# Performance work log

Measured on AMD Instinct MI355X. Metric: run time of the kernel, lower is better.

Reference implementation:

```python
import jax, jax.numpy as jnp
import numpy as np
from jax import lax

DIM = 256
POS = 32
RATIO = 4
LN_EPS = 1e-5


def _layernorm(x, g, b):
    m = x.mean(-1, keepdims=True)
    v = ((x - m) ** 2).mean(-1, keepdims=True)
    return (x - m) * lax.rsqrt(v + LN_EPS) * g + b


def _pos_embed(pos, h, w):
    # pos: [1, C, POS, POS] -> bilinear (align_corners=False / half-pixel) -> [1, h*w, C]
    p = jax.image.resize(pos, (1, pos.shape[1], h, w), method='bilinear')
    return p.transpose(0, 2, 3, 1).reshape(1, h * w, pos.shape[1])


def _scan_branch(u, ln_g, ln_b, Wf, bf, Ww, bw, Wo, bo):
    # u: [B, N, C]. Pooled LN context -> concat gates -> gated linear recurrence.
    c = _layernorm(u.mean(1), ln_g, ln_b)                       # [B, C]
    z = jnp.concatenate([u, jnp.broadcast_to(c[:, None, :], u.shape)], -1)
    d = jax.nn.softplus(z @ Wf + bf)
    g = jax.nn.sigmoid(z @ Ww + bw)
    o = jax.nn.sigmoid(z @ Wo + bo)
    a = jnp.exp(-d)
    b = (1.0 - a) * (g * u)

    def step(s, t):
        a_t, b_t, o_t, u_t = t
        s = a_t * s + b_t
        return s, o_t * s + (1.0 - o_t) * u_t

    xs = tuple(jnp.swapaxes(v, 0, 1) for v in (a, b, o, u))     # [N, B, C]
    s0 = jnp.zeros((u.shape[0], u.shape[2]), u.dtype)
    _, y = lax.scan(step, s0, xs)
    return jnp.swapaxes(y, 0, 1)                                # [B, N, C]


def setup_inputs() -> dict:
    key = jax.random.key(0)
    ks = jax.random.split(key, 32)
    d = DIM

    def W(k, i, o, s=0.02):
        return (jax.random.normal(k, (i, o), jnp.float32) * s)

    inp = {
        'x': jax.random.normal(ks[0], (8, d, 64, 64), jnp.float32),
        'Wt': W(ks[1], d, d), 'bt': jnp.zeros((d,), jnp.float32),
        'pos_fine': jax.random.normal(ks[2], (1, d, POS, POS), jnp.float32) * 0.02,
        'pos_glob': jax.random.normal(ks[3], (1, d, POS, POS), jnp.float32) * 0.02,
        'ln_g': jnp.ones((d,), jnp.float32), 'ln_b': jnp.zeros((d,), jnp.float32),
        'Wf': W(ks[4], 2 * d, d), 'bf': jnp.zeros((d,), jnp.float32),
        'Ww': W(ks[5], 2 * d, d), 'bw': jnp.zeros((d,), jnp.float32),
        'Wo': W(ks[6], 2 * d, d), 'bo': jnp.zeros((d,), jnp.float32),
        'Wr': W(ks[7], 3 * d, d), 'br': jnp.zeros((d,), jnp.float32),
        'Wgi': W(ks[8], 3 * d, d), 'bgi': jnp.zeros((d,), jnp.float32),
        'dw_w': jax.random.normal(ks[9], (d, 1, 3, 3), jnp.float32) * 0.1,
        'dw_b': jnp.zeros((d,), jnp.float32),
        'Wl': W(ks[10], d, d), 'bl': jnp.zeros((d,), jnp.float32),
        'Wlf': W(ks[11], 2 * d, d), 'blf': jnp.zeros((d,), jnp.float32),
        'Wout': W(ks[12], d, d), 'bout': jnp.zeros((d,), jnp.float32),
    }
    return inp


def reference(x, Wt, bt, pos_fine, pos_glob, ln_g, ln_b, Wf, bf, Ww, bw, Wo, bo,
              Wr, br, Wgi, bgi, dw_w, dw_b, Wl, bl, Wlf, blf, Wout, bout):
    bsz, c, h, w = x.shape
    gate_params = (ln_g, ln_b, Wf, bf, Ww, bw, Wo, bo)

    # fine sequence: token proj + interpolated learnable pos
    seq = x.transpose(0, 2, 3, 1).reshape(bsz, h * w, c)
    u = seq @ Wt + bt + _pos_embed(pos_fine, h, w)

    # bidirectional gated scan
    y_f = _scan_branch(u, *gate_params)
    y_b = jnp.flip(_scan_branch(jnp.flip(u, 1), *gate_params), 1)
    rho = jax.nn.sigmoid(jnp.concatenate([u, y_f, y_b], -1) @ Wr + br)
    y = rho * y_f + (1.0 - rho) * y_b

    # global branch: exact avg pool (H,W divisible by RATIO) -> scan -> upsample
    gh, gw = h // RATIO, w // RATIO
    x_g = x.reshape(bsz, c, gh, RATIO, gw, RATIO).mean((3, 5))
    seq_g = x_g.transpose(0, 2, 3, 1).reshape(bsz, gh * gw, c)
    u_g = seq_g @ Wt + bt + _pos_embed(pos_glob, gh, gw)
    y_g = _scan_branch(u_g, *gate_params)
    y_g_map = y_g.reshape(bsz, gh, gw, c).transpose(0, 3, 1, 2)
    y_g_up = jax.image.resize(y_g_map, (bsz, c, h, w), method='bilinear')
    y_g_seq = y_g_up.transpose(0, 2, 3, 1).reshape(bsz, h * w, c)

    lam = jax.nn.sigmoid(jnp.concatenate([y, y_g_seq, u], -1) @ Wgi + bgi)
    z = y + lam * y_g_seq

    # local depthwise conv branch
    v_map = lax.conv_general_dilated(x, dw_w, (1, 1), 'SAME',
                                     feature_group_count=c) + dw_b[None, :, None, None]
    v = v_map.transpose(0, 2, 3, 1).reshape(bsz, h * w, c) @ Wl + bl
    eta = jax.nn.sigmoid(jnp.concatenate([v, z], -1) @ Wlf + blf)
    u_out = eta * v + (1.0 - eta) * z

    # 1x1 conv output proj + residual
    out_map = (u_out @ Wout + bout).reshape(bsz, h, w, c).transpose(0, 3, 1, 2)
    return x + out_map
```

## Files before the change

### kernel.cpp

```cpp
#include <hip/hip_runtime.h>
#include <cstddef>

#define B_  8
#define C_  256
#define H_  64
#define W_  64
#define HW_ 4096
#define NG_ 256

typedef unsigned short u16;
typedef __attribute__((ext_vector_type(8))) short short8;
typedef __attribute__((ext_vector_type(4))) float f32x4;

__device__ __forceinline__ float sigm(float v) { return 1.f / (1.f + expf(-v)); }

__device__ __forceinline__ u16 f2bf(float f) {
    union { float f; unsigned u; } x; x.f = f;
    unsigned r = x.u + 0x7fff + ((x.u >> 16) & 1);
    return (u16)(r >> 16);
}
__device__ __forceinline__ float bf2f(u16 h) {
    union { unsigned u; float f; } x; x.u = ((unsigned)h) << 16;
    return x.f;
}

__global__ __launch_bounds__(256) void prepw_k(
    const float* __restrict__ Wt, const float* __restrict__ Wf, const float* __restrict__ Ww,
    const float* __restrict__ Wo, const float* __restrict__ Wr, const float* __restrict__ Wgi,
    const float* __restrict__ Wl, const float* __restrict__ Wlf, const float* __restrict__ Wout,
    u16* __restrict__ Wpre)
{
    int s = blockIdx.z;
    const float* Wsrc; int rowoff = 0;
    switch (s) {
        case 0: Wsrc = Wt; break;
        case 1: Wsrc = Wf; break;
        case 2: Wsrc = Ww; break;
        case 3: Wsrc = Wo; break;
        case 4: case 5: case 6: Wsrc = Wr;  rowoff = (s - 4) * 256; break;
        case 7: case 8: case 9: Wsrc = Wgi; rowoff = (s - 7) * 256; break;
        case 10: Wsrc = Wl; break;
        case 11: case 12: Wsrc = Wlf; rowoff = (s - 11) * 256; break;
        default: Wsrc = Wout; break;
    }
    __shared__ float t[32][33];
    int k0 = blockIdx.y * 32, n0 = blockIdx.x * 32;
    int tx = threadIdx.x, ty = threadIdx.y;
#pragma unroll
    for (int i = 0; i < 32; i += 8)
        t[ty + i][tx] = Wsrc[(size_t)(rowoff + k0 + ty + i) * 256 + n0 + tx];
    __syncthreads();
    u16* op = Wpre + (size_t)s * 65536;
#pragma unroll
    for (int i = 0; i < 32; i += 8)
        op[(size_t)(n0 + ty + i) * 256 + k0 + tx] = f2bf(t[tx][ty + i]);
}

#define LDK 72
__global__ __launch_bounds__(256, 4) void gemm_bf16(
    const u16* __restrict__ A0, const u16* __restrict__ A1, const u16* __restrict__ A2,
    int nseg, const u16* __restrict__ Wpre, const float* __restrict__ bias,
    const float* __restrict__ pos, const float* __restrict__ aux0,
    const u16* __restrict__ auxb0, const u16* __restrict__ auxb1,
    float* __restrict__ out, u16* __restrict__ out2, int NTOK, int mode)
{
    __shared__ u16 Asm[64 * LDK];
    __shared__ u16 Bsm[128 * LDK];
    const int tid = threadIdx.x;
    const int lane = tid & 63, wave = tid >> 6;
    const int wm = wave & 1, wn = wave >> 1;
    const int m0 = blockIdx.x * 64, n0 = blockIdx.y * 128;
    const int l15 = lane & 15, lq = lane >> 4;

    f32x4 acc[2][4] = {};

    const int rowA = tid >> 2, kA = (tid & 3) * 16;
    const int rowB = tid >> 1, kB = (tid & 1) * 32;

    for (int seg = 0; seg < nseg; ++seg) {
        const u16* __restrict__ A = (seg == 0) ? A0 : ((seg == 1) ? A1 : A2);
        const u16* arow = A + (size_t)(m0 + rowA) * 256 + kA;
        const u16* wrow = Wpre + (size_t)seg * 65536 + (size_t)(n0 + rowB) * 256 + kB;

        for (int k0 = 0; k0 < 256; k0 += 64) {
            *(short8*)(&Asm[rowA * LDK + kA])     = *(const short8*)(arow + k0);
            *(short8*)(&Asm[rowA * LDK + kA + 8]) = *(const short8*)(arow + k0 + 8);
#pragma unroll
            for (int c = 0; c < 4; ++c)
                *(short8*)(&Bsm[rowB * LDK + kB + c * 8]) =
                    *(const short8*)(wrow + k0 + c * 8);
            __syncthreads();

#pragma unroll
            for (int ks = 0; ks < 2; ++ks) {
                short8 af[2], bfr[4];
#pragma unroll
                for (int i = 0; i < 2; ++i)
                    af[i] = *(const short8*)(&Asm[(wm * 32 + i * 16 + l15) * LDK + ks * 32 + lq * 8]);
#pragma unroll
                for (int j = 0; j < 4; ++j)
                    bfr[j] = *(const short8*)(&Bsm[(wn * 64 + j * 16 + l15) * LDK + ks * 32 + lq * 8]);
#pragma unroll
                for (int i = 0; i < 2; ++i)
#pragma unroll
                    for (int j = 0; j < 4; ++j)
                        acc[i][j] = __builtin_amdgcn_mfma_f32_16x16x32_bf16(
                            af[i], bfr[j], acc[i][j], 0, 0, 0);
            }
            __syncthreads();
        }
    }

#pragma unroll
    for (int i = 0; i < 2; ++i) {
        int mbase = m0 + wm * 32 + i * 16 + lq * 4;
#pragma unroll
        for (int j = 0; j < 4; ++j) {
            int n = n0 + wn * 64 + j * 16 + l15;
            if (mode == 9) {
                int b9 = mbase >> 12, hw = mbase & 4095;
                size_t oi = ((size_t)b9 * 256 + n) * 4096 + hw;
                float bn = bias[n];
                float4 xr = *(const float4*)(aux0 + oi);
                float4 res;
                res.x = xr.x + acc[i][j][0] + bn;
                res.y = xr.y + acc[i][j][1] + bn;
                res.z = xr.z + acc[i][j][2] + bn;
                res.w = xr.w + acc[i][j][3] + bn;
                *(float4*)(out + oi) = res;
                continue;
            }
            float bn = bias[n];
#pragma unroll
            for (int r = 0; r < 4; ++r) {
                int m = mbase + r;
                size_t idx = (size_t)m * 256 + n;
                float D = acc[i][j][r] + bn;
                if (mode == 1) {
                    float v = D + pos[(size_t)(m % NTOK) * 256 + n];
                    out[idx] = v; out2[idx] = f2bf(v);
                } else if (mode == 10) {
                    float v = D + pos[(size_t)(m % NTOK) * 256 + n];
                    out2[idx] = f2bf(v);
                } else if (mode == 11) {
                    float r_ = sigm(D);
                    out2[idx] = f2bf(r_ * bf2f(auxb0[idx]) + (1.f - r_) * bf2f(auxb1[idx]));
                } else if (mode == 6) {
                    float l = sigm(D);
                    out2[idx] = f2bf(bf2f(auxb1[idx]) + l * bf2f(auxb0[idx]));
                } else if (mode == 7) {
                    out2[idx] = f2bf(D);
                } else {
                    float e = sigm(D);
                    out2[idx] = f2bf(e * bf2f(auxb0[idx]) + (1.f - e) * bf2f(auxb1[idx]));
                }
            }
        }
    }
}

__global__ __launch_bounds__(256, 4) void gemm_gates3(
    const u16* __restrict__ A0, const u16* __restrict__ Wg, const float* __restrict__ cf,
    const u16* __restrict__ ubf, float* __restrict__ aF, float* __restrict__ bbF,
    u16* __restrict__ obf, int NTOK)
{
    __shared__ u16 Asm[64 * LDK];
    __shared__ u16 Bsm[3][64 * LDK];
    const int tid = threadIdx.x;
    const int lane = tid & 63, wave = tid >> 6;
    const int wm = wave & 1, wn = wave >> 1;
    const int m0 = blockIdx.x * 64, n0 = blockIdx.y * 64;
    const int l15 = lane & 15, lq = lane >> 4;

    f32x4 acc[3][2][2] = {};

    const int rowA = tid >> 2, kA = (tid & 3) * 16;
    const u16* arow = A0 + (size_t)(m0 + rowA) * 256 + kA;
    const u16* wrow = Wg + (size_t)(n0 + rowA) * 256 + kA;

    for (int k0 = 0; k0 < 256; k0 += 64) {
        *(short8*)(&Asm[rowA * LDK + kA])     = *(const short8*)(arow + k0);
        *(short8*)(&Asm[rowA * LDK + kA + 8]) = *(const short8*)(arow + k0 + 8);
#pragma unroll
        for (int ws = 0; ws < 3; ++ws) {
            const u16* wr = wrow + (size_t)ws * 65536 + k0;
            *(short8*)(&Bsm[ws][rowA * LDK + kA])     = *(const short8*)(wr);
            *(short8*)(&Bsm[ws][rowA * LDK + kA + 8]) = *(const short8*)(wr + 8);
        }
        __syncthreads();
#pragma unroll
        for (int ks = 0; ks < 2; ++ks) {
            short8 af[2];
#pragma unroll
            for (int i = 0; i < 2; ++i)
                af[i] = *(const short8*)(&Asm[(wm * 32 + i * 16 + l15) * LDK + ks * 32 + lq * 8]);
#pragma unroll
            for (int ws = 0; ws < 3; ++ws) {
                short8 bfr[2];
#pragma unroll
                for (int j = 0; j < 2; ++j)
                    bfr[j] = *(const short8*)(&Bsm[ws][(wn * 32 + j * 16 + l15) * LDK + ks * 32 + lq * 8]);
#pragma unroll
                for (int i = 0; i < 2; ++i)
#pragma unroll
                    for (int j = 0; j < 2; ++j)
                        acc[ws][i][j] = __builtin_amdgcn_mfma_f32_16x16x32_bf16(
                            af[i], bfr[j], acc[ws][i][j], 0, 0, 0);
            }
        }
        __syncthreads();
    }

#pragma unroll
    for (int i = 0; i < 2; ++i) {
        int mbase = m0 + wm * 32 + i * 16 + lq * 4;
        int bt_ = mbase / NTOK;
#pragma unroll
        for (int j = 0; j < 2; ++j) {
            int n = n0 + wn * 32 + j * 16 + l15;
            float cD = cf[((size_t)0 * B_ + bt_) * C_ + n];
            float cW = cf[((size_t)1 * B_ + bt_) * C_ + n];
            float cO = cf[((size_t)2 * B_ + bt_) * C_ + n];
#pragma unroll
            for (int r = 0; r < 4; ++r) {
                size_t idx = (size_t)(mbase + r) * 256 + n;
                float a_ = sigm(-(acc[0][i][j][r] + cD));
                float g_ = sigm(acc[1][i][j][r] + cW);
                float o_ = sigm(acc[2][i][j][r] + cO);
                float u_ = bf2f(ubf[idx]);
                aF[idx]  = a_;
                bbF[idx] = (1.f - a_) * g_ * u_;
                obf[idx] = f2bf(o_);
            }
        }
    }
}

__global__ __launch_bounds__(256) void transpose_bf_k(const float* __restrict__ in,
                                                      u16* __restrict__ outb)
{
    __shared__ float t[32][33];
    int b = blockIdx.z;
    int r0 = blockIdx.y * 32, c0 = blockIdx.x * 32;
    int tx = threadIdx.x, ty = threadIdx.y;
    const float* ip = in + (size_t)b * HW_ * C_;
    u16* op = outb + (size_t)b * HW_ * C_;
#pragma unroll
    for (int k = 0; k < 32; k += 8)
        t[ty + k][tx] = ip[(size_t)(r0 + ty + k) * HW_ + c0 + tx];
    __syncthreads();
#pragma unroll
    for (int k = 0; k < 32; k += 8)
        op[(size_t)(c0 + ty + k) * C_ + r0 + tx] = f2bf(t[tx][ty + k]);
}

__global__ __launch_bounds__(256) void dwconvt3_k(const float* __restrict__ x,
                                                  const float* __restrict__ dww,
                                                  const float* __restrict__ dwb,
                                                  u16* __restrict__ vseq)
{
    __shared__ float sx[32 * 384];
    __shared__ float sw[32 * 9];
    __shared__ float sb[32];
    const int t = threadIdx.x;
    const int l   = (blockIdx.x & 7) * 128 + (blockIdx.x >> 3);
    const int hch = l & 15;
    const int chb = (l >> 4) & 7;
    const int b   = l >> 7;
    const int r0 = chb * 32, h0 = hch * 4;

    for (int p = t; p < 288; p += 256) sw[p] = dww[(size_t)(r0 + p / 9) * 9 + p % 9];
    if (t < 32) sb[t] = dwb[r0 + t];

    const float* xb = x + (size_t)(b * 256 + r0) * 4096;
#pragma unroll
    for (int j = 0; j < 12; ++j) {
        int seg = j * 256 + t;
        int ch  = seg / 96;
        int r4  = seg - ch * 96;
        int rr  = r4 >> 4;
        int w4  = (r4 & 15) * 4;
        int hh  = h0 - 1 + rr;
        float4 v = make_float4(0.f, 0.f, 0.f, 0.f);
        if (hh >= 0 && hh <= 63)
            v = *(const float4*)(xb + (size_t)ch * 4096 + hh * 64 + w4);
        *(float4*)(&sx[seg * 4]) = v;
    }
    __syncthreads();

    const int w = t & 63, chq = t >> 6;
    float res[4][8];
#pragma unroll
    for (int i = 0; i < 8; ++i) {
        const int ch = chq * 8 + i;
        const float* cw = &sw[ch * 9];
        const float* bp = &sx[ch * 384 + w];
        float aa[4];
        aa[0] = aa[1] = aa[2] = aa[3] = sb[ch];
#pragma unroll
        for (int rr = 0; rr < 6; ++rr) {
            const float* rp = bp + rr * 64;
            float cc = rp[0];
            float lf = (w > 0)  ? rp[-1] : 0.f;
            float rt = (w < 63) ? rp[1]  : 0.f;
            if (rr < 4)            aa[rr]     += lf * cw[0] + cc * cw[1] + rt * cw[2];
            if (rr >= 1 && rr < 5) aa[rr - 1] += lf * cw[3] + cc * cw[4] + rt * cw[5];
            if (rr >= 2)           aa[rr - 2] += lf * cw[6] + cc * cw[7] + rt * cw[8];
        }
#pragma unroll
        for (int r = 0; r < 4; ++r) res[r][i] = aa[r];
    }

    size_t obase = ((size_t)b * HW_ + (size_t)(h0 * 64 + w)) * 256 + r0 + chq * 8;
#pragma unroll
    for (int r = 0; r < 4; ++r) {
        short8 v;
#pragma unroll
        for (int i = 0; i < 8; ++i) v[i] = (short)f2bf(res[r][i]);
        *(short8*)(vseq + obase + (size_t)r * 64 * 256) = v;
    }
}

__global__ __launch_bounds__(256) void pool_k(const float* __restrict__ x, u16* __restrict__ seqg)
{
    int b = blockIdx.x, c = blockIdx.y, ghw = threadIdx.x;
    int gh = ghw >> 4, gw = ghw & 15;
    const float* xp = x + ((size_t)b * C_ + c) * HW_;
    float s = 0.f;
#pragma unroll
    for (int dy = 0; dy < 4; ++dy)
#pragma unroll
        for (int dx = 0; dx < 4; ++dx)
            s += xp[(gh * 4 + dy) * W_ + gw * 4 + dx];
    seqg[((size_t)b * NG_ + ghw) * C_ + c] = f2bf(s * (1.f / 16.f));
}

__global__ __launch_bounds__(256) void posfine_k(const float* __restrict__ pf, float* __restrict__ posF)
{
    int hw = blockIdx.x, c = threadIdx.x;
    int h = hw >> 6, w = hw & 63;
    float fy = h * 0.5f - 0.25f, fx = w * 0.5f - 0.25f;
    int y0 = (int)floorf(fy); float wy = fy - (float)y0;
    int x0 = (int)floorf(fx); float wx = fx - (float)x0;
    int y0c = min(max(y0, 0), 31), y1c = min(max(y0 + 1, 0), 31);
    int x0c = min(max(x0, 0), 31), x1c = min(max(x0 + 1, 0), 31);
    const float* p = pf + (size_t)c * 1024;
    float v = (1.f - wy) * ((1.f - wx) * p[y0c * 32 + x0c] + wx * p[y0c * 32 + x1c])
            +        wy  * ((1.f - wx) * p[y1c * 32 + x0c] + wx * p[y1c * 32 + x1c]);
    posF[(size_t)hw * C_ + c] = v;
}

__global__ __launch_bounds__(256) void posglob_k(const float* __restrict__ pg, float* __restrict__ posG)
{
    int ghw = blockIdx.x, c = threadIdx.x;
    int gh = ghw >> 4, gw = ghw & 15;
    const float wt[4] = {0.125f, 0.375f, 0.375f, 0.125f};
    float wy[4], wx[4]; int jy[4], jx[4];
    float sy = 0.f, sx = 0.f;
#pragma unroll
    for (int k = 0; k < 4; ++k) {
        jy[k] = 2 * gh - 1 + k; jx[k] = 2 * gw - 1 + k;
        wy[k] = (jy[k] >= 0 && jy[k] < 32) ? wt[k] : 0.f; sy += wy[k];
        wx[k] = (jx[k] >= 0 && jx[k] < 32) ? wt[k] : 0.f; sx += wx[k];
    }
    const float* p = pg + (size_t)c * 1024;
    float acc = 0.f;
#pragma unroll
    for (int ky = 0; ky < 4; ++ky) {
        if (wy[ky] == 0.f) continue;
        float row = 0.f;
#pragma unroll
        for (int kx = 0; kx < 4; ++kx)
            if (wx[kx] != 0.f) row += wx[kx] * p[jy[ky] * 32 + jx[kx]];
        acc += wy[ky] * row;
    }
    posG[(size_t)ghw * C_ + c] = acc / (sy * sx);
}

__global__ __launch_bounds__(256) void upsample_k(const float* __restrict__ yg, u16* __restrict__ ygs)
{
    int b = blockIdx.x >> 12, hw = blockIdx.x & 4095, c = threadIdx.x;
    int h = hw >> 6, w = hw & 63;
    float fy = h * 0.25f - 0.375f, fx = w * 0.25f - 0.375f;
    int y0 = (int)floorf(fy); float wy = fy - (float)y0;
    int x0 = (int)floorf(fx); float wx = fx - (float)x0;
    int y0c = min(max(y0, 0), 15), y1c = min(max(y0 + 1, 0), 15);
    int x0c = min(max(x0, 0), 15), x1c = min(max(x0 + 1, 0), 15);
    const float* p = yg + (size_t)b * NG_ * C_ + c;
    float v = (1.f - wy) * ((1.f - wx) * p[(y0c * 16 + x0c) * C_] + wx * p[(y0c * 16 + x1c) * C_])
            +        wy  * ((1.f - wx) * p[(y1c * 16 + x0c) * C_] + wx * p[(y1c * 16 + x1c) * C_]);
    ygs[((size_t)b * HW_ + hw) * C_ + c] = f2bf(v);
}

__global__ __launch_bounds__(256) void meanpart_k(const float* __restrict__ u, float* __restrict__ part,
                                                  int Ntok, int chunkLen)
{
    int b = blockIdx.x, s = blockIdx.y, c = threadIdx.x;
    float acc = 0.f;
    for (int i = 0; i < chunkLen; ++i) {
        int t = s * chunkLen + i;
        acc += u[((size_t)b * Ntok + t) * C_ + c];
    }
    part[((size_t)b * gridDim.y + s) * C_ + c] = acc;
}

__global__ __launch_bounds__(256) void meanpart_bf_k(const u16* __restrict__ u, float* __restrict__ part,
                                                     int Ntok, int chunkLen)
{
    int b = blockIdx.x, s = blockIdx.y, c = threadIdx.x;
    float acc = 0.f;
    for (int i = 0; i < chunkLen; ++i) {
        int t = s * chunkLen + i;
        acc += bf2f(u[((size_t)b * Ntok + t) * C_ + c]);
    }
    part[((size_t)b * gridDim.y + s) * C_ + c] = acc;
}

__global__ __launch_bounds__(256) void ln_k(const float* __restrict__ part, int S, float invN,
                                            const float* __restrict__ g, const float* __restrict__ bta,
                                            float* __restrict__ cout)
{
    __shared__ float red[256];
    int c = threadIdx.x, b = blockIdx.x;
    float v = 0.f;
    for (int s = 0; s < S; ++s) v += part[((size_t)b * S + s) * C_ + c];
    v *= invN;
    red[c] = v; __syncthreads();
    for (int st = 128; st > 0; st >>= 1) { if (c < st) red[c] += red[c + st]; __syncthreads(); }
    float m = red[0] * (1.f / 256.f);
    __syncthreads();
    float d = v - m;
    red[c] = d * d; __syncthreads();
    for (int st = 128; st > 0; st >>= 1) { if (c < st) red[c] += red[c + st]; __syncthreads(); }
    float var = red[0] * (1.f / 256.f);
    cout[(size_t)b * C_ + c] = d * rsqrtf(var + 1e-5f) * g[c] + bta[c];
}

__global__ __launch_bounds__(256) void gatebias_k(const float* __restrict__ cvec,
    const float* __restrict__ Wf, const float* __restrict__ bf,
    const float* __restrict__ Ww, const float* __restrict__ bw,
    const float* __restrict__ Wo, const float* __restrict__ bo,
    float* __restrict__ outb)
{
    int n = threadIdx.x, b = blockIdx.x, gate = blockIdx.y;
    const float* Wm = (gate == 0) ? Wf : ((gate == 1) ? Ww : Wo);
    const float* bi = (gate == 0) ? bf : ((gate == 1) ? bw : bo);
    __shared__ float cs[256];
    cs[n] = cvec[(size_t)b * C_ + n];
    __syncthreads();
    float acc = bi[n];
    for (int k = 0; k < 256; ++k)
        acc += cs[k] * Wm[(size_t)(256 + k) * C_ + n];
    outb[((size_t)gate * B_ + b) * C_ + n] = acc;
}

__global__ __launch_bounds__(256) void scan_p1b(
    const float* __restrict__ a, const float* __restrict__ bb,
    float* __restrict__ AbF, float* __restrict__ BbF,
    float* __restrict__ AbB, float* __restrict__ BbB,
    int Ntok, int nchunk, int both)
{
    int c = threadIdx.x;
    int ch = blockIdx.x % nchunk;
    int b = blockIdx.x / nchunk;
    int CL = Ntok / nchunk;
    size_t base = ((size_t)b * Ntok + (size_t)ch * CL) * C_ + c;
    float sA = 1.f, sB = 0.f;
    for (int i = 0; i < CL; ++i) {
        float av = a[base + (size_t)i * C_];
        sB = av * sB + bb[base + (size_t)i * C_];
        sA *= av;
    }
    size_t o = ((size_t)b * nchunk + ch) * C_ + c;
    AbF[o] = sA; BbF[o] = sB;
    if (both) {
        sA = 1.f; sB = 0.f;
        for (int i = CL - 1; i >= 0; --i) {
            float av = a[base + (size_t)i * C_];
            sB = av * sB + bb[base + (size_t)i * C_];
            sA *= av;
        }
        size_t ob = ((size_t)b * nchunk + (nchunk - 1 - ch)) * C_ + c;
        AbB[ob] = sA; BbB[ob] = sB;
    }
}

__global__ __launch_bounds__(256) void scan_p2b(
    const float* __restrict__ AbF, const float* __restrict__ BbF, float* __restrict__ SbF,
    const float* __restrict__ AbB, const float* __restrict__ BbB, float* __restrict__ SbB,
    int nchunk, int both)
{
    int c = threadIdx.x, b = blockIdx.x;
    float s = 0.f;
    for (int ch = 0; ch < nchunk; ++ch) {
        size_t o = ((size_t)b * nchunk + ch) * C_ + c;
        SbF[o] = s;
        s = AbF[o] * s + BbF[o];
    }
    if (both) {
        s = 0.f;
        for (int ch = 0; ch < nchunk; ++ch) {
            size_t o = ((size_t)b * nchunk + ch) * C_ + c;
            SbB[o] = s;
            s = AbB[o] * s + BbB[o];
        }
    }
}

__global__ __launch_bounds__(256) void scan_p3b(
    const float* __restrict__ a, const float* __restrict__ bb,
    const u16* __restrict__ obf, const u16* __restrict__ ubf,
    const float* __restrict__ SbF, const float* __restrict__ SbB,
    float* __restrict__ yout, u16* __restrict__ ybfF, u16* __restrict__ ybfB,
    int Ntok, int nchunk, int both)
{
    int c = threadIdx.x;
    int ch = blockIdx.x % nchunk;
    int b = blockIdx.x / nchunk;
    int CL = Ntok / nchunk;
    size_t base = ((size_t)b * Ntok + (size_t)ch * CL) * C_ + c;
    float s = SbF[((size_t)b * nchunk + ch) * C_ + c];
    for (int i = 0; i < CL; ++i) {
        size_t idx = base + (size_t)i * C_;
        float av = a[idx];
        s = av * s + bb[idx];
        float ov = bf2f(obf[idx]);
        float y = ov * s + (1.f - ov) * bf2f(ubf[idx]);
        if (yout) yout[idx] = y;
        if (ybfF) ybfF[idx] = f2bf(y);
    }
    if (both) {
        float sb = SbB[((size_t)b * nchunk + (nchunk - 1 - ch)) * C_ + c];
        for (int i = CL - 1; i >= 0; --i) {
            size_t idx = base + (size_t)i * C_;
            float av = a[idx];
            sb = av * sb + bb[idx];
            float ov = bf2f(obf[idx]);
            ybfB[idx] = f2bf(ov * sb + (1.f - ov) * bf2f(ubf[idx]));
        }
    }
}

extern "C" void kernel_launch(void* const* d_in, const int* in_sizes, int n_in,
                              void* d_out, int out_size, void* d_ws, size_t ws_size,
                              hipStream_t stream)
{
    const float* x        = (const float*)d_in[0];
    const float* Wt       = (const float*)d_in[1];
    const float* bt       = (const float*)d_in[2];
    const float* pos_fine = (const float*)d_in[3];
    const float* pos_glob = (const float*)d_in[4];
    const float* ln_g     = (const float*)d_in[5];
    const float* ln_b     = (const float*)d_in[6];
    const float* Wf       = (const float*)d_in[7];
    const float* bf       = (const float*)d_in[8];
    const float* Ww       = (const float*)d_in[9];
    const float* bw       = (const float*)d_in[10];
    const float* Wo       = (const float*)d_in[11];
    const float* bo       = (const float*)d_in[12];
    const float* Wr       = (const float*)d_in[13];
    const float* br       = (const float*)d_in[14];
    const float* Wgi      = (const float*)d_in[15];
    const float* bgi      = (const float*)d_in[16];
    const float* dww      = (const float*)d_in[17];
    const float* dwb      = (const float*)d_in[18];
    const float* Wl       = (const float*)d_in[19];
    const float* bl       = (const float*)d_in[20];
    const float* Wlf      = (const float*)d_in[21];
    const float* blf      = (const float*)d_in[22];
    const float* Wout     = (const float*)d_in[23];
    const float* bout     = (const float*)d_in[24];
    float* out = (float*)d_out;

    float* w = (float*)d_ws;
    const size_t BNC = (size_t)B_ * HW_ * C_;
    float* bu  = w + 0 * BNC;
    float* ba  = w + 1 * BNC;
    float* bbb = w + 2 * BNC;
    float* bo_ = w + 3 * BNC;
    u16* bf1 = (u16*)(w + 4 * BNC);
    u16* bf2 = bf1 + BNC;
    u16* bf3 = bf2 + BNC;
    u16* bf4 = bf3 + BNC;
    u16* bf5 = bf4 + BNC;
    float* ext = w + 4 * BNC + 5 * (BNC / 2);
    float* posF = ext;  ext += (size_t)HW_ * C_;
    float* posG = ext;  ext += (size_t)NG_ * C_;
    float* part = ext;  ext += (size_t)B_ * 32 * C_;
    float* cln  = ext;  ext += (size_t)B_ * C_;
    float* cf   = ext;  ext += (size_t)3 * B_ * C_;
    float* ug   = ext;  ext += (size_t)B_ * NG_ * C_;
    float* ag   = ext;  ext += (size_t)B_ * NG_ * C_;
    float* bbg  = ext;  ext += (size_t)B_ * NG_ * C_;
    float* ygt  = ext;  ext += (size_t)B_ * NG_ * C_;
    float* chAF = ext;  ext += (size_t)B_ * 64 * C_;
    float* chBF = ext;  ext += (size_t)B_ * 64 * C_;
    float* chSF = ext;  ext += (size_t)B_ * 64 * C_;
    u16* seqg_bf = (u16*)ext;  ext += (size_t)B_ * NG_ * C_ / 2;
    u16* ug_bf   = (u16*)ext;  ext += (size_t)B_ * NG_ * C_ / 2;
    u16* og_bf   = (u16*)ext;  ext += (size_t)B_ * NG_ * C_ / 2;
    u16* Wpre    = (u16*)ext;
    float* chAB = bu;
    float* chBB = bu + (size_t)B_ * 64 * C_;
    float* chSB = bu + (size_t)2 * B_ * 64 * C_;
    u16* obf    = (u16*)bo_;

    const dim3 blk256(256);
    const dim3 blkT(32, 8);
    const dim3 gBig(B_ * HW_ / 64, 2);
    const dim3 gSml(B_ * NG_ / 64, 2);
    const dim3 gGateF(B_ * HW_ / 64, 4);
    const dim3 gGateG(B_ * NG_ / 64, 4);
    const size_t WS = 65536;
    const float *F0 = nullptr; const u16 *U0 = nullptr;
    float *FW = nullptr; u16 *UW = nullptr;

    prepw_k<<<dim3(8, 8, 14), blkT, 0, stream>>>(Wt, Wf, Ww, Wo, Wr, Wgi, Wl, Wlf, Wout, Wpre);

    transpose_bf_k<<<dim3(HW_ / 32, C_ / 32, B_), blkT, 0, stream>>>(x, bf1);
    posfine_k<<<HW_, blk256, 0, stream>>>(pos_fine, posF);
    gemm_bf16<<<gBig, blk256, 0, stream>>>(bf1, U0, U0, 1, Wpre + 0 * WS, bt,
        posF, F0, U0, U0, FW, bf2, HW_, 10);

    pool_k<<<dim3(B_, C_), blk256, 0, stream>>>(x, seqg_bf);
    posglob_k<<<NG_, blk256, 0, stream>>>(pos_glob, posG);
    gemm_bf16<<<gSml, blk256, 0, stream>>>(seqg_bf, U0, U0, 1, Wpre + 0 * WS, bt,
        posG, F0, U0, U0, ug, ug_bf, NG_, 1);
    meanpart_k<<<dim3(B_, 8), blk256, 0, stream>>>(ug, part, NG_, 32);
    ln_k<<<B_, blk256, 0, stream>>>(part, 8, 1.f / NG_, ln_g, ln_b, cln);
    gatebias_k<<<dim3(B_, 3), blk256, 0, stream>>>(cln, Wf, bf, Ww, bw, Wo, bo, cf);
    gemm_gates3<<<gGateG, blk256, 0, stream>>>(ug_bf, Wpre + 1 * WS, cf, ug_bf,
        ag, bbg, og_bf, NG_);
    scan_p1b<<<B_ * 16, blk256, 0, stream>>>(ag, bbg, chAF, chBF, FW, FW, NG_, 16, 0);
    scan_p2b<<<B_, blk256, 0, stream>>>(chAF, chBF, chSF, F0, F0, FW, 16, 0);
    scan_p3b<<<B_ * 16, blk256, 0, stream>>>(ag, bbg, og_bf, ug_bf, chSF, F0,
        ygt, UW, UW, NG_, 16, 0);
    upsample_k<<<B_ * HW_, blk256, 0, stream>>>(ygt, bf5);

    meanpart_bf_k<<<dim3(B_, 32), blk256, 0, stream>>>(bf2, part, HW_, 128);
    ln_k<<<B_, blk256, 0, stream>>>(part, 32, 1.f / HW_, ln_g, ln_b, cln);
    gatebias_k<<<dim3(B_, 3), blk256, 0, stream>>>(cln, Wf, bf, Ww, bw, Wo, bo, cf);
    gemm_gates3<<<gGateF, blk256, 0, stream>>>(bf2, Wpre + 1 * WS, cf, bf2,
        ba, bbb, obf, HW_);
    scan_p1b<<<B_ * 64, blk256, 0, stream>>>(ba, bbb, chAF, chBF, chAB, chBB, HW_, 64, 1);
    scan_p2b<<<B_, blk256, 0, stream>>>(chAF, chBF, chSF, chAB, chBB, chSB, 64, 1);
    scan_p3b<<<B_ * 64, blk256, 0, stream>>>(ba, bbb, obf, bf2, chSF, chSB,
        FW, bf1, bf3, HW_, 64, 1);

    gemm_bf16<<<gBig, blk256, 0, stream>>>(bf2, bf1, bf3, 3, Wpre + 4 * WS, br,
        F0, F0, bf1, bf3, FW, bf4, HW_, 11);

    gemm_bf16<<<gBig, blk256, 0, stream>>>(bf4, bf5, bf2, 3, Wpre + 7 * WS, bgi,
        F0, F0, bf5, bf4, FW, bf1, HW_, 6);

    dwconvt3_k<<<dim3(1024), blk256, 0, stream>>>(x, dww, dwb, bf3);
    gemm_bf16<<<gBig, blk256, 0, stream>>>(bf3, U0, U0, 1, Wpre + 10 * WS, bl,
        F0, F0, U0, U0, FW, bf2, HW_, 7);
    gemm_bf16<<<gBig, blk256, 0, stream>>>(bf2, bf1, U0, 2, Wpre + 11 * WS, blf,
        F0, F0, bf2, bf1, FW, bf3, HW_, 8);

    gemm_bf16<<<gBig, blk256, 0, stream>>>(bf3, U0, U0, 1, Wpre + 13 * WS, bout,
        F0, x, U0, U0, out, UW, HW_, 9);
}
```

Measured before the change: 641.8 us.

## Raise scan chunk count and parallelize forward/backward carry pass with prefetch

The fine-scale scan now uses 256 chunks instead of 64, so phases 1 and 3 launch four times as many blocks with shorter serial chains. The carry-propagation kernel runs the forward and backward directions in two halves of a 512-thread block and software-prefetches chunk summaries in groups of 8. The chunk buffers are moved into a larger scratch region. In exchange, the serial phase-2 chain becomes longer, and the new kernel assumes nchunk is a multiple of 8.

```diff
diff --git a/kernel.cpp b/kernel.cpp
--- a/kernel.cpp
+++ b/kernel.cpp
@@ -485,25 +485,42 @@
     }
 }
 
-__global__ __launch_bounds__(256) void scan_p2b(
+__global__ __launch_bounds__(512) void scan_p2c(
     const float* __restrict__ AbF, const float* __restrict__ BbF, float* __restrict__ SbF,
     const float* __restrict__ AbB, const float* __restrict__ BbB, float* __restrict__ SbB,
     int nchunk, int both)
 {
-    int c = threadIdx.x, b = blockIdx.x;
+    const int c = threadIdx.x & 255, half = threadIdx.x >> 8, b = blockIdx.x;
+    if (half && !both) return;
+    const float* __restrict__ Ap = half ? AbB : AbF;
+    const float* __restrict__ Bp = half ? BbB : BbF;
+    float* __restrict__       Sp = half ? SbB : SbF;
+    const size_t base = (size_t)b * nchunk * C_ + c;
+    float a0[8], b0[8], a1[8], b1[8];
+#pragma unroll
+    for (int j = 0; j < 8; ++j) {
+        a0[j] = Ap[base + (size_t)j * C_];
+        b0[j] = Bp[base + (size_t)j * C_];
+    }
     float s = 0.f;
-    for (int ch = 0; ch < nchunk; ++ch) {
-        size_t o = ((size_t)b * nchunk + ch) * C_ + c;
-        SbF[o] = s;
-        s = AbF[o] * s + BbF[o];
-    }
-    if (both) {
-        s = 0.f;
-        for (int ch = 0; ch < nchunk; ++ch) {
-            size_t o = ((size_t)b * nchunk + ch) * C_ + c;
-            SbB[o] = s;
-            s = AbB[o] * s + BbB[o];
-        }
+    const int nb = nchunk >> 3;
+    for (int t = 0; t < nb; ++t) {
+        const size_t nbase = base + (size_t)(t + 1) * 8 * C_;
+        if (t + 1 < nb) {
+#pragma unroll
+            for (int j = 0; j < 8; ++j) {
+                a1[j] = Ap[nbase + (size_t)j * C_];
+                b1[j] = Bp[nbase + (size_t)j * C_];
+            }
+        }
+        const size_t cbase = base + (size_t)t * 8 * C_;
+#pragma unroll
+        for (int j = 0; j < 8; ++j) {
+            Sp[cbase + (size_t)j * C_] = s;
+            s = a0[j] * s + b0[j];
+        }
+#pragma unroll
+        for (int j = 0; j < 8; ++j) { a0[j] = a1[j]; b0[j] = b1[j]; }
     }
 }
 
@@ -593,16 +610,17 @@
     float* ag   = ext;  ext += (size_t)B_ * NG_ * C_;
     float* bbg  = ext;  ext += (size_t)B_ * NG_ * C_;
     float* ygt  = ext;  ext += (size_t)B_ * NG_ * C_;
-    float* chAF = ext;  ext += (size_t)B_ * 64 * C_;
-    float* chBF = ext;  ext += (size_t)B_ * 64 * C_;
-    float* chSF = ext;  ext += (size_t)B_ * 64 * C_;
     u16* seqg_bf = (u16*)ext;  ext += (size_t)B_ * NG_ * C_ / 2;
     u16* ug_bf   = (u16*)ext;  ext += (size_t)B_ * NG_ * C_ / 2;
     u16* og_bf   = (u16*)ext;  ext += (size_t)B_ * NG_ * C_ / 2;
     u16* Wpre    = (u16*)ext;
-    float* chAB = bu;
-    float* chBB = bu + (size_t)B_ * 64 * C_;
-    float* chSB = bu + (size_t)2 * B_ * 64 * C_;
+    const size_t CHS = (size_t)B_ * 256 * C_;
+    float* chAF = bu + 0 * CHS;
+    float* chBF = bu + 1 * CHS;
+    float* chSF = bu + 2 * CHS;
+    float* chAB = bu + 3 * CHS;
+    float* chBB = bu + 4 * CHS;
+    float* chSB = bu + 5 * CHS;
     u16* obf    = (u16*)bo_;
 
     const dim3 blk256(256);
@@ -612,6 +630,8 @@
     const dim3 gGateF(B_ * HW_ / 64, 4);
     const dim3 gGateG(B_ * NG_ / 64, 4);
     const size_t WS = 65536;
+    const int NCH_F = 256;
+    const int NCH_G = 16;
     const float *F0 = nullptr; const u16 *U0 = nullptr;
     float *FW = nullptr; u16 *UW = nullptr;
 
@@ -631,10 +651,10 @@
     gatebias_k<<<dim3(B_, 3), blk256, 0, stream>>>(cln, Wf, bf, Ww, bw, Wo, bo, cf);
     gemm_gates3<<<gGateG, blk256, 0, stream>>>(ug_bf, Wpre + 1 * WS, cf, ug_bf,
         ag, bbg, og_bf, NG_);
-    scan_p1b<<<B_ * 16, blk256, 0, stream>>>(ag, bbg, chAF, chBF, FW, FW, NG_, 16, 0);
-    scan_p2b<<<B_, blk256, 0, stream>>>(chAF, chBF, chSF, F0, F0, FW, 16, 0);
-    scan_p3b<<<B_ * 16, blk256, 0, stream>>>(ag, bbg, og_bf, ug_bf, chSF, F0,
-        ygt, UW, UW, NG_, 16, 0);
+    scan_p1b<<<B_ * NCH_G, blk256, 0, stream>>>(ag, bbg, chAF, chBF, FW, FW, NG_, NCH_G, 0);
+    scan_p2c<<<B_, dim3(512), 0, stream>>>(chAF, chBF, chSF, F0, F0, FW, NCH_G, 0);
+    scan_p3b<<<B_ * NCH_G, blk256, 0, stream>>>(ag, bbg, og_bf, ug_bf, chSF, F0,
+        ygt, UW, UW, NG_, NCH_G, 0);
     upsample_k<<<B_ * HW_, blk256, 0, stream>>>(ygt, bf5);
 
     meanpart_bf_k<<<dim3(B_, 32), blk256, 0, stream>>>(bf2, part, HW_, 128);
@@ -642,10 +662,10 @@
     gatebias_k<<<dim3(B_, 3), blk256, 0, stream>>>(cln, Wf, bf, Ww, bw, Wo, bo, cf);
     gemm_gates3<<<gGateF, blk256, 0, stream>>>(bf2, Wpre + 1 * WS, cf, bf2,
         ba, bbb, obf, HW_);
-    scan_p1b<<<B_ * 64, blk256, 0, stream>>>(ba, bbb, chAF, chBF, chAB, chBB, HW_, 64, 1);
-    scan_p2b<<<B_, blk256, 0, stream>>>(chAF, chBF, chSF, chAB, chBB, chSB, 64, 1);
-    scan_p3b<<<B_ * 64, blk256, 0, stream>>>(ba, bbb, obf, bf2, chSF, chSB,
-        FW, bf1, bf3, HW_, 64, 1);
+    scan_p1b<<<B_ * NCH_F, blk256, 0, stream>>>(ba, bbb, chAF, chBF, chAB, chBB, HW_, NCH_F, 1);
+    scan_p2c<<<B_, dim3(512), 0, stream>>>(chAF, chBF, chSF, chAB, chBB, chSB, NCH_F, 1);
+    scan_p3b<<<B_ * NCH_F, blk256, 0, stream>>>(ba, bbb, obf, bf2, chSF, chSB,
+        FW, bf1, bf3, HW_, NCH_F, 1);
 
     gemm_bf16<<<gBig, blk256, 0, stream>>>(bf2, bf1, bf3, 3, Wpre + 4 * WS, br,
         F0, F0, bf1, bf3, FW, bf4, HW_, 11);
```

Result: faster. 596.0 us (-7.1%).
